# Kernel optimization log

Measured on AMD Instinct MI355X. Metric: run time of the kernel, lower is better.

The kernel has to match this reference:

```python
import jax, jax.numpy as jnp
import numpy as np

N_BASIS = 16


def _kan_layer(x, coeffs, centers):
    # x: [b, in], coeffs: [out, in, n], centers: [n]
    mu = jnp.mean(x, axis=0)
    sd = jnp.std(x, axis=0, ddof=1)  # torch.std is unbiased by default
    xn = jnp.clip((x - mu) / (sd + 1e-6), -3.0, 3.0)
    # Gaussian RBF expansion: [b, in, n]
    basis = jnp.exp(-((xn[..., None] - centers) ** 2) / 0.5)
    return jnp.einsum('bin,oin->bo', basis, coeffs)


def setup_inputs() -> dict:
    key = jax.random.key(0)
    ks = jax.random.split(key, 6)
    B, IN, H = 16384, 256, 512
    return {
        'x': jax.random.normal(ks[0], (B, IN), jnp.float32),
        'coeffs1': jax.random.normal(ks[1], (H, IN, N_BASIS), jnp.float32) * 0.1,
        'coeffs2': jax.random.normal(ks[2], (H, H, N_BASIS), jnp.float32) * 0.1,
        'coeffs3': jax.random.normal(ks[3], (1, H, N_BASIS), jnp.float32) * 0.1,
        'skip_w': jax.random.normal(ks[4], (1, IN), jnp.float32) * 0.05,
        'skip_b': jnp.zeros((1,), jnp.float32),
    }


def reference(x, coeffs1, coeffs2, coeffs3, skip_w, skip_b):
    centers = jnp.linspace(-2.0, 2.0, N_BASIS).astype(x.dtype)
    h = jnp.tanh(_kan_layer(x, coeffs1, centers))
    h = jnp.tanh(_kan_layer(h, coeffs2, centers))
    out = _kan_layer(h, coeffs3, centers)[:, 0]  # squeeze(-1)
    skip = (x @ skip_w.T + skip_b)[:, 0]
    return out + skip
```

## Files before the change

kernel.cpp:

```cpp
#include <hip/hip_runtime.h>
#include <cstdint>
#include <cstddef>

typedef __attribute__((ext_vector_type(8))) _Float16 half8;
typedef __attribute__((ext_vector_type(4))) _Float16 half4;
typedef __attribute__((ext_vector_type(4))) float    floatx4;

static constexpr int B_ROWS = 16384;
static constexpr int IN_DIM = 256;
static constexpr int H_DIM  = 512;
static constexpr int NB     = 16;

__device__ __forceinline__ float fast_tanh(float x) {
  float ax = fabsf(x);
  float e  = __expf(2.0f * ax);
  float t  = 1.0f - 2.0f / (e + 1.0f);
  return copysignf(t, x);
}

__device__ __forceinline__ void gld16(const void* g, void* l) {
  __builtin_amdgcn_global_load_lds(
      (const __attribute__((address_space(1))) unsigned int*)g,
      (__attribute__((address_space(3))) unsigned int*)l, 16, 0, 0);
}

__global__ __launch_bounds__(256) void prep_k(const float* __restrict__ c1, _Float16* __restrict__ d1, size_t n41,
                                              const float* __restrict__ c2, _Float16* __restrict__ d2, size_t n42,
                                              const float* __restrict__ X,
                                              float* __restrict__ ps, float* __restrict__ ps2) {
  const int bx = blockIdx.x;
  if (bx < 128) {
    int c     = (bx & 3) * 64 + (threadIdx.x & 63);
    int chunk = threadIdx.x >> 6;
    int seg   = bx >> 2;
    int r0    = seg * 512;
    double s = 0.0, s2 = 0.0;
    for (int r = r0 + chunk; r < r0 + 512; r += 4) {
      float v = X[(size_t)r * IN_DIM + c];
      s += v; s2 += (double)v * (double)v;
    }
    __shared__ float Ls[256], Ls2[256];
    Ls[threadIdx.x] = (float)s; Ls2[threadIdx.x] = (float)s2;
    __syncthreads();
    if (chunk == 0) {
      int cl = threadIdx.x;
      float a  = Ls[cl]  + Ls[cl + 64]  + Ls[cl + 128]  + Ls[cl + 192];
      float b  = Ls2[cl] + Ls2[cl + 64] + Ls2[cl + 128] + Ls2[cl + 192];
      ps [(size_t)seg * IN_DIM + c] = a;
      ps2[(size_t)seg * IN_DIM + c] = b;
    }
  } else {
    size_t tot = n41 + n42;
    int nb_blocks = gridDim.x - 128;
    for (size_t i = (size_t)(bx - 128) * 256 + threadIdx.x; i < tot;
         i += (size_t)nb_blocks * 256) {
      const float4* sp; half4* dp; size_t j;
      if (i < n41) { sp = (const float4*)c1; dp = (half4*)d1; j = i; }
      else         { sp = (const float4*)c2; dp = (half4*)d2; j = i - n41; }
      float4 v = sp[j];
      int nb = (int)((j << 2) & 15);
      half4 r;
      float e0 = -2.f + (float)(nb + 0) * (4.f / 15.f);
      float e1 = -2.f + (float)(nb + 1) * (4.f / 15.f);
      float e2 = -2.f + (float)(nb + 2) * (4.f / 15.f);
      float e3 = -2.f + (float)(nb + 3) * (4.f / 15.f);
      r[0] = (_Float16)(v.x * __expf(-2.f * e0 * e0));
      r[1] = (_Float16)(v.y * __expf(-2.f * e1 * e1));
      r[2] = (_Float16)(v.z * __expf(-2.f * e2 * e2));
      r[3] = (_Float16)(v.w * __expf(-2.f * e3 * e3));
      dp[j] = r;
    }
  }
}

__global__ void stats_final_k(const float* __restrict__ ps,
                              const float* __restrict__ ps2,
                              int segs, int cols, int rows,
                              float* __restrict__ mu, float* __restrict__ isd) {
  int c = blockIdx.x * blockDim.x + threadIdx.x;
  if (c >= cols) return;
  double s = 0.0, s2 = 0.0;
  for (int g = 0; g < segs; g++) { s += ps[(size_t)g * cols + c]; s2 += ps2[(size_t)g * cols + c]; }
  double mean = s / rows;
  double var  = (s2 - s * s / rows) / (rows - 1);
  if (var < 0.0) var = 0.0;
  float sd = (float)sqrt(var);
  mu[c]  = (float)mean;
  isd[c] = 1.0f / (sd + 1e-6f);
}

__global__ __launch_bounds__(256, 2) void kan_gemm_fused(const float* __restrict__ X,
                                                         const float* __restrict__ mu,
                                                         const float* __restrict__ isd,
                                                         const _Float16* __restrict__ Bm,
                                                         float* __restrict__ Hout,
                                                         float* __restrict__ psum,
                                                         float* __restrict__ psum2,
                                                         int C) {
  const int K = C << 4;
  const int steps = K >> 6;
  __shared__ __align__(16) _Float16 As[2][128 * 64];
  __shared__ __align__(16) _Float16 Bs[2][128 * 64];
  __shared__ float Rs1[2][128], Rs2[2][128];
  const int tid  = threadIdx.x;
  const int w = tid >> 6, lane = tid & 63;
  const int wm = w & 1, wn = w >> 1;
  const int lrow = lane & 15, quad = lane >> 4;
  const int row0 = blockIdx.x * 128;
  const int col0 = blockIdx.y * 128;

  const int s_row = tid >> 3;
  const int s_sl  = tid & 7;
  const int s_seg = s_sl ^ ((s_row >> 1) & 7);
  const _Float16* gB = Bm + (size_t)(col0 + s_row) * K + s_seg * 8;

  const int erow = tid >> 1, eh = tid & 1;
  const float* xp  = X   + (size_t)(row0 + erow) * C + 2 * eh;
  const float* mup = mu  + 2 * eh;
  const float* isp = isd + 2 * eh;

  floatx4 acc[4][4] = {};

  auto expand_store = [&](float2 v, float2 m, float2 sdi, int bufi) {
#pragma unroll
    for (int h = 0; h < 2; h++) {
      float xr = h ? v.y : v.x;
      float mm = h ? m.y : m.x;
      float ii = h ? sdi.y : sdi.x;
      float xn = fminf(fmaxf((xr - mm) * ii, -3.f), 3.f);
      float Wv = __expf(-2.f * xn * xn - 8.f * xn);
      float g  = __expf((16.f / 15.f) * xn);
      half8 h0, h1;
      float p = Wv;
#pragma unroll
      for (int n = 0; n < 8; n++) { h0[n] = (_Float16)p; p *= g; }
#pragma unroll
      for (int n = 0; n < 8; n++) { h1[n] = (_Float16)p; p *= g; }
      int ks0 = 4 * eh + 2 * h;
      *(half8*)&As[bufi][(size_t)(ks0 * 128 + erow) * 8]       = h0;
      *(half8*)&As[bufi][(size_t)((ks0 + 1) * 128 + erow) * 8] = h1;
    }
  };

#pragma unroll
  for (int i = 0; i < 4; i++)
    gld16(gB + (size_t)32 * i * K, &Bs[0][(size_t)(tid + 256 * i) * 8]);
  expand_store(*(const float2*)xp, *(const float2*)mup, *(const float2*)isp, 0);
  float2 xv = {}, mv = {}, iv = {};
  if (steps > 1) {
    xv = *(const float2*)(xp + 4);
    mv = *(const float2*)(mup + 4);
    iv = *(const float2*)(isp + 4);
  }
  __syncthreads();

  for (int k = 0; k < steps; k++) {
    const int buf = k & 1, nb = buf ^ 1;
    if (k + 1 < steps) {
#pragma unroll
      for (int i = 0; i < 4; i++)
        gld16(gB + (size_t)(k + 1) * 64 + (size_t)32 * i * K,
              &Bs[nb][(size_t)(tid + 256 * i) * 8]);
      expand_store(xv, mv, iv, nb);
      if (k + 2 < steps) {
        xv = *(const float2*)(xp + 4 * (k + 2));
        mv = *(const float2*)(mup + 4 * (k + 2));
        iv = *(const float2*)(isp + 4 * (k + 2));
      }
    }
    __builtin_amdgcn_s_setprio(1);
#pragma unroll
    for (int ks = 0; ks < 2; ks++) {
      half8 af[4], bf[4];
#pragma unroll
      for (int t = 0; t < 4; t++) {
        int arow = wm * 64 + t * 16 + lrow;
        af[t] = *(const half8*)&As[buf][(size_t)((4 * ks + quad) * 128 + arow) * 8];
        int brow = wn * 64 + t * 16 + lrow;
        int bchunk = brow * 8 + ((4 * ks + quad) ^ ((brow >> 1) & 7));
        bf[t] = *(const half8*)&Bs[buf][(size_t)bchunk * 8];
      }
#pragma unroll
      for (int tm = 0; tm < 4; tm++)
#pragma unroll
        for (int tn = 0; tn < 4; tn++)
          acc[tm][tn] = __builtin_amdgcn_mfma_f32_16x16x32_f16(af[tm], bf[tn], acc[tm][tn], 0, 0, 0);
    }
    __builtin_amdgcn_s_setprio(0);
    __syncthreads();
  }

  float s1[4] = {0.f, 0.f, 0.f, 0.f}, s2v[4] = {0.f, 0.f, 0.f, 0.f};
#pragma unroll
  for (int tm = 0; tm < 4; tm++) {
#pragma unroll
    for (int tn = 0; tn < 4; tn++) {
      int gcol = col0 + wn * 64 + tn * 16 + lrow;
#pragma unroll
      for (int r = 0; r < 4; r++) {
        int grow = row0 + wm * 64 + tm * 16 + quad * 4 + r;
        float v = fast_tanh(acc[tm][tn][r]);
        Hout[(size_t)grow * H_DIM + gcol] = v;
        s1[tn] += v; s2v[tn] += v * v;
      }
    }
  }
#pragma unroll
  for (int tn = 0; tn < 4; tn++) {
    s1[tn]  += __shfl_xor(s1[tn], 16);  s1[tn]  += __shfl_xor(s1[tn], 32);
    s2v[tn] += __shfl_xor(s2v[tn], 16); s2v[tn] += __shfl_xor(s2v[tn], 32);
  }
  if (quad == 0) {
#pragma unroll
    for (int tn = 0; tn < 4; tn++) {
      Rs1[wm][wn * 64 + tn * 16 + lrow] = s1[tn];
      Rs2[wm][wn * 64 + tn * 16 + lrow] = s2v[tn];
    }
  }
  __syncthreads();
  if (tid < 128) {
    psum [(size_t)blockIdx.x * H_DIM + col0 + tid] = Rs1[0][tid] + Rs1[1][tid];
    psum2[(size_t)blockIdx.x * H_DIM + col0 + tid] = Rs2[0][tid] + Rs2[1][tid];
  }
}

__global__ __launch_bounds__(256) void layer3_k(const float* __restrict__ H2,
                                                const float* __restrict__ mu,
                                                const float* __restrict__ isd,
                                                const float* __restrict__ C3,
                                                const float* __restrict__ X,
                                                const float* __restrict__ SW,
                                                const float* __restrict__ SB,
                                                float* __restrict__ OUT) {
  int w = threadIdx.x >> 6, lane = threadIdx.x & 63;
  float Kn[NB];
#pragma unroll
  for (int n = 0; n < NB; n++) {
    float c = -2.f + (float)n * (4.f / 15.f);
    Kn[n] = __expf(-2.f * c * c);
  }
  float sb0 = SB[0];
  int row_base = blockIdx.x * 16 + w * 4;
  for (int r = 0; r < 4; r++) {
    int row = row_base + r;
    float s = 0.f;
#pragma unroll
    for (int j = 0; j < 8; j++) {
      int i = lane + 64 * j;
      float hv = H2[(size_t)row * H_DIM + i];
      float xn = fminf(fmaxf((hv - mu[i]) * isd[i], -3.f), 3.f);
      float Wf = __expf(-2.f * xn * xn - 8.f * xn);
      float gf = __expf((16.f / 15.f) * xn);
      const floatx4* cp = (const floatx4*)(C3 + (size_t)i * NB);
      floatx4 c0 = cp[0], c1 = cp[1], c2 = cp[2], c3 = cp[3];
      float p = Wf;
#pragma unroll
      for (int n = 0; n < 4; n++) { s += p * Kn[n]      * c0[n]; p *= gf; }
#pragma unroll
      for (int n = 0; n < 4; n++) { s += p * Kn[n + 4]  * c1[n]; p *= gf; }
#pragma unroll
      for (int n = 0; n < 4; n++) { s += p * Kn[n + 8]  * c2[n]; p *= gf; }
#pragma unroll
      for (int n = 0; n < 4; n++) { s += p * Kn[n + 12] * c3[n]; p *= gf; }
    }
#pragma unroll
    for (int j = 0; j < 4; j++) {
      int i = lane + 64 * j;
      s += X[(size_t)row * IN_DIM + i] * SW[i];
    }
#pragma unroll
    for (int off = 32; off > 0; off >>= 1) s += __shfl_down(s, off);
    if (lane == 0) OUT[row] = s + sb0;
  }
}

extern "C" void kernel_launch(void* const* d_in, const int* in_sizes, int n_in,
                              void* d_out, int out_size, void* d_ws, size_t ws_size,
                              hipStream_t stream) {
  const float* x  = (const float*)d_in[0];
  const float* c1 = (const float*)d_in[1];
  const float* c2 = (const float*)d_in[2];
  const float* c3 = (const float*)d_in[3];
  const float* sw = (const float*)d_in[4];
  const float* sb = (const float*)d_in[5];
  float* out = (float*)d_out;

  const int B = B_ROWS, IN = IN_DIM, H = H_DIM;

  char* ws = (char*)d_ws;
  size_t off = 0;
  auto alloc = [&](size_t bytes) -> void* {
    void* p = ws + off;
    off += (bytes + 255) & ~(size_t)255;
    return p;
  };
  _Float16* C1h = (_Float16*)alloc((size_t)H * IN * NB * 2);
  _Float16* C2h = (_Float16*)alloc((size_t)H * H  * NB * 2);
  float* H1 = (float*)alloc((size_t)B * H * 4);
  float* H2 = (float*)alloc((size_t)B * H * 4);
  float* ps  = (float*)alloc(128 * 512 * 4);
  float* ps2 = (float*)alloc(128 * 512 * 4);
  float* mu  = (float*)alloc(512 * 4);
  float* isd = (float*)alloc(512 * 4);

  prep_k<<<128 + 1024, 256, 0, stream>>>(c1, C1h, (size_t)H * IN * NB / 4,
                                         c2, C2h, (size_t)H * H * NB / 4,
                                         x, ps, ps2);
  stats_final_k<<<1, 256, 0, stream>>>(ps, ps2, 32, IN, B, mu, isd);

  kan_gemm_fused<<<dim3(B / 128, 4), 256, 0, stream>>>(x, mu, isd, C1h, H1, ps, ps2, IN);
  stats_final_k<<<2, 256, 0, stream>>>(ps, ps2, 128, H, B, mu, isd);

  kan_gemm_fused<<<dim3(B / 128, 4), 256, 0, stream>>>(H1, mu, isd, C2h, H2, ps, ps2, H);
  stats_final_k<<<2, 256, 0, stream>>>(ps, ps2, 128, H, B, mu, isd);

  layer3_k<<<B / 16, 256, 0, stream>>>(H2, mu, isd, c3, x, sw, sb, out);
}
```

Measured before the change: 474.5 us.

## Interleave RBF expansion between MFMA halves and use packed fp16 power chain

```diff
diff --git a/kernel.cpp b/kernel.cpp
--- a/kernel.cpp
+++ b/kernel.cpp
@@ -4,6 +4,7 @@
 
 typedef __attribute__((ext_vector_type(8))) _Float16 half8;
 typedef __attribute__((ext_vector_type(4))) _Float16 half4;
+typedef __attribute__((ext_vector_type(2))) __fp16   fp16x2;
 typedef __attribute__((ext_vector_type(4))) float    floatx4;
 
 static constexpr int B_ROWS = 16384;
@@ -76,7 +77,7 @@
 __global__ void stats_final_k(const float* __restrict__ ps,
                               const float* __restrict__ ps2,
                               int segs, int cols, int rows,
-                              float* __restrict__ mu, float* __restrict__ isd) {
+                              float* __restrict__ nmi, float* __restrict__ isd) {
   int c = blockIdx.x * blockDim.x + threadIdx.x;
   if (c >= cols) return;
   double s = 0.0, s2 = 0.0;
@@ -85,12 +86,13 @@
   double var  = (s2 - s * s / rows) / (rows - 1);
   if (var < 0.0) var = 0.0;
   float sd = (float)sqrt(var);
-  mu[c]  = (float)mean;
-  isd[c] = 1.0f / (sd + 1e-6f);
+  float iv = 1.0f / (sd + 1e-6f);
+  isd[c] = iv;
+  nmi[c] = -(float)mean * iv;
 }
 
 __global__ __launch_bounds__(256, 2) void kan_gemm_fused(const float* __restrict__ X,
-                                                         const float* __restrict__ mu,
+                                                         const float* __restrict__ nmi,
                                                          const float* __restrict__ isd,
                                                          const _Float16* __restrict__ Bm,
                                                          float* __restrict__ Hout,
@@ -116,76 +118,98 @@
 
   const int erow = tid >> 1, eh = tid & 1;
   const float* xp  = X   + (size_t)(row0 + erow) * C + 2 * eh;
-  const float* mup = mu  + 2 * eh;
+  const float* mup = nmi + 2 * eh;
   const float* isp = isd + 2 * eh;
 
   floatx4 acc[4][4] = {};
 
-  auto expand_store = [&](float2 v, float2 m, float2 sdi, int bufi) {
+  auto expand_store = [&](float2 v, float2 a, float2 b, int bufi) {
 #pragma unroll
     for (int h = 0; h < 2; h++) {
       float xr = h ? v.y : v.x;
-      float mm = h ? m.y : m.x;
-      float ii = h ? sdi.y : sdi.x;
-      float xn = fminf(fmaxf((xr - mm) * ii, -3.f), 3.f);
-      float Wv = __expf(-2.f * xn * xn - 8.f * xn);
+      float ii = h ? a.y : a.x;
+      float bb = h ? b.y : b.x;
+      float xn = fminf(fmaxf(fmaf(xr, ii, bb), -3.f), 3.f);
+      float Wv = __expf(fmaf(-2.f, xn, -8.f) * xn);
       float g  = __expf((16.f / 15.f) * xn);
-      half8 h0, h1;
-      float p = Wv;
-#pragma unroll
-      for (int n = 0; n < 8; n++) { h0[n] = (_Float16)p; p *= g; }
-#pragma unroll
-      for (int n = 0; n < 8; n++) { h1[n] = (_Float16)p; p *= g; }
+      float g2 = g * g, g4 = g2 * g2, g8 = g4 * g4;
+      fp16x2 gg = __builtin_amdgcn_cvt_pkrtz(g2, g2);
+      union { fp16x2 q[4]; half8 v8; } u0, u1;
+      u0.q[0] = __builtin_amdgcn_cvt_pkrtz(Wv, Wv * g);
+      u0.q[1] = u0.q[0] * gg;
+      u0.q[2] = u0.q[1] * gg;
+      u0.q[3] = u0.q[2] * gg;
+      float W8 = Wv * g8;
+      u1.q[0] = __builtin_amdgcn_cvt_pkrtz(W8, W8 * g);
+      u1.q[1] = u1.q[0] * gg;
+      u1.q[2] = u1.q[1] * gg;
+      u1.q[3] = u1.q[2] * gg;
       int ks0 = 4 * eh + 2 * h;
-      *(half8*)&As[bufi][(size_t)(ks0 * 128 + erow) * 8]       = h0;
-      *(half8*)&As[bufi][(size_t)((ks0 + 1) * 128 + erow) * 8] = h1;
+      *(half8*)&As[bufi][(size_t)(ks0 * 128 + erow) * 8]       = u0.v8;
+      *(half8*)&As[bufi][(size_t)((ks0 + 1) * 128 + erow) * 8] = u1.v8;
     }
   };
 
 #pragma unroll
   for (int i = 0; i < 4; i++)
     gld16(gB + (size_t)32 * i * K, &Bs[0][(size_t)(tid + 256 * i) * 8]);
-  expand_store(*(const float2*)xp, *(const float2*)mup, *(const float2*)isp, 0);
-  float2 xv = {}, mv = {}, iv = {};
+  expand_store(*(const float2*)xp, *(const float2*)isp, *(const float2*)mup, 0);
+  float2 xv = {}, av = {}, bv = {};
   if (steps > 1) {
     xv = *(const float2*)(xp + 4);
-    mv = *(const float2*)(mup + 4);
-    iv = *(const float2*)(isp + 4);
+    av = *(const float2*)(isp + 4);
+    bv = *(const float2*)(mup + 4);
   }
   __syncthreads();
 
   for (int k = 0; k < steps; k++) {
     const int buf = k & 1, nb = buf ^ 1;
-    if (k + 1 < steps) {
+    const bool more = (k + 1 < steps);
+    if (more) {
 #pragma unroll
       for (int i = 0; i < 4; i++)
         gld16(gB + (size_t)(k + 1) * 64 + (size_t)32 * i * K,
               &Bs[nb][(size_t)(tid + 256 * i) * 8]);
-      expand_store(xv, mv, iv, nb);
+    }
+    half8 af0[4], bf0[4];
+#pragma unroll
+    for (int t = 0; t < 4; t++) {
+      int arow = wm * 64 + t * 16 + lrow;
+      af0[t] = *(const half8*)&As[buf][(size_t)(quad * 128 + arow) * 8];
+      int brow = wn * 64 + t * 16 + lrow;
+      int bchunk = brow * 8 + (quad ^ ((brow >> 1) & 7));
+      bf0[t] = *(const half8*)&Bs[buf][(size_t)bchunk * 8];
+    }
+    __builtin_amdgcn_s_setprio(1);
+#pragma unroll
+    for (int tm = 0; tm < 4; tm++)
+#pragma unroll
+      for (int tn = 0; tn < 4; tn++)
+        acc[tm][tn] = __builtin_amdgcn_mfma_f32_16x16x32_f16(af0[tm], bf0[tn], acc[tm][tn], 0, 0, 0);
+    __builtin_amdgcn_s_setprio(0);
+    if (more) {
+      expand_store(xv, av, bv, nb);
       if (k + 2 < steps) {
         xv = *(const float2*)(xp + 4 * (k + 2));
-        mv = *(const float2*)(mup + 4 * (k + 2));
-        iv = *(const float2*)(isp + 4 * (k + 2));
+        av = *(const float2*)(isp + 4 * (k + 2));
+        bv = *(const float2*)(mup + 4 * (k + 2));
       }
     }
+    half8 af1[4], bf1[4];
+#pragma unroll
+    for (int t = 0; t < 4; t++) {
+      int arow = wm * 64 + t * 16 + lrow;
+      af1[t] = *(const half8*)&As[buf][(size_t)((4 + quad) * 128 + arow) * 8];
+      int brow = wn * 64 + t * 16 + lrow;
+      int bchunk = brow * 8 + ((4 + quad) ^ ((brow >> 1) & 7));
+      bf1[t] = *(const half8*)&Bs[buf][(size_t)bchunk * 8];
+    }
     __builtin_amdgcn_s_setprio(1);
 #pragma unroll
-    for (int ks = 0; ks < 2; ks++) {
-      half8 af[4], bf[4];
-#pragma unroll
-      for (int t = 0; t < 4; t++) {
-        int arow = wm * 64 + t * 16 + lrow;
-        af[t] = *(const half8*)&As[buf][(size_t)((4 * ks + quad) * 128 + arow) * 8];
-        int brow = wn * 64 + t * 16 + lrow;
-        int bchunk = brow * 8 + ((4 * ks + quad) ^ ((brow >> 1) & 7));
-        bf[t] = *(const half8*)&Bs[buf][(size_t)bchunk * 8];
-      }
-#pragma unroll
-      for (int tm = 0; tm < 4; tm++)
-#pragma unroll
-        for (int tn = 0; tn < 4; tn++)
-          acc[tm][tn] = __builtin_amdgcn_mfma_f32_16x16x32_f16(af[tm], bf[tn], acc[tm][tn], 0, 0, 0);
-    }
+    for (int tm = 0; tm < 4; tm++)
+#pragma unroll
+      for (int tn = 0; tn < 4; tn++)
+        acc[tm][tn] = __builtin_amdgcn_mfma_f32_16x16x32_f16(af1[tm], bf1[tn], acc[tm][tn], 0, 0, 0);
     __builtin_amdgcn_s_setprio(0);
     __syncthreads();
   }
@@ -225,7 +249,7 @@
 }
 
 __global__ __launch_bounds__(256) void layer3_k(const float* __restrict__ H2,
-                                                const float* __restrict__ mu,
+                                                const float* __restrict__ nmi,
                                                 const float* __restrict__ isd,
                                                 const float* __restrict__ C3,
                                                 const float* __restrict__ X,
@@ -248,8 +272,8 @@
     for (int j = 0; j < 8; j++) {
       int i = lane + 64 * j;
       float hv = H2[(size_t)row * H_DIM + i];
-      float xn = fminf(fmaxf((hv - mu[i]) * isd[i], -3.f), 3.f);
-      float Wf = __expf(-2.f * xn * xn - 8.f * xn);
+      float xn = fminf(fmaxf(fmaf(hv, isd[i], nmi[i]), -3.f), 3.f);
+      float Wf = __expf(fmaf(-2.f, xn, -8.f) * xn);
       float gf = __expf((16.f / 15.f) * xn);
       const floatx4* cp = (const floatx4*)(C3 + (size_t)i * NB);
       floatx4 c0 = cp[0], c1 = cp[1], c2 = cp[2], c3 = cp[3];
@@ -300,19 +324,19 @@
   float* H2 = (float*)alloc((size_t)B * H * 4);
   float* ps  = (float*)alloc(128 * 512 * 4);
   float* ps2 = (float*)alloc(128 * 512 * 4);
-  float* mu  = (float*)alloc(512 * 4);
+  float* nmi = (float*)alloc(512 * 4);
   float* isd = (float*)alloc(512 * 4);
 
   prep_k<<<128 + 1024, 256, 0, stream>>>(c1, C1h, (size_t)H * IN * NB / 4,
                                          c2, C2h, (size_t)H * H * NB / 4,
                                          x, ps, ps2);
-  stats_final_k<<<1, 256, 0, stream>>>(ps, ps2, 32, IN, B, mu, isd);
-
-  kan_gemm_fused<<<dim3(B / 128, 4), 256, 0, stream>>>(x, mu, isd, C1h, H1, ps, ps2, IN);
-  stats_final_k<<<2, 256, 0, stream>>>(ps, ps2, 128, H, B, mu, isd);
-
-  kan_gemm_fused<<<dim3(B / 128, 4), 256, 0, stream>>>(H1, mu, isd, C2h, H2, ps, ps2, H);
-  stats_final_k<<<2, 256, 0, stream>>>(ps, ps2, 128, H, B, mu, isd);
-
-  layer3_k<<<B / 16, 256, 0, stream>>>(H2, mu, isd, c3, x, sw, sb, out);
-}
+  stats_final_k<<<1, 256, 0, stream>>>(ps, ps2, 32, IN, B, nmi, isd);
+
+  kan_gemm_fused<<<dim3(B / 128, 4), 256, 0, stream>>>(x, nmi, isd, C1h, H1, ps, ps2, IN);
+  stats_final_k<<<2, 256, 0, stream>>>(ps, ps2, 128, H, B, nmi, isd);
+
+  kan_gemm_fused<<<dim3(B / 128, 4), 256, 0, stream>>>(H1, nmi, isd, C2h, H2, ps, ps2, H);
+  stats_final_k<<<2, 256, 0, stream>>>(ps, ps2, 128, H, B, nmi, isd);
+
+  layer3_k<<<B / 16, 256, 0, stream>>>(H2, nmi, isd, c3, x, sw, sb, out);
+}
```

After: 455.6 us. 1.04x faster.
